# Kernel optimization log

Measured on AMD Instinct MI355X. Metric: run time of the kernel, lower is better.

## Reference

```python
import jax, jax.numpy as jnp
import numpy as np

N_NODES = 100000
D_FEAT = 128
UNITS = 128
N_EDGES = 600000


def setup_inputs() -> dict:
    key = jax.random.key(0)
    k1, k2, k3, k4, k5 = jax.random.split(key, 5)
    X = jax.random.normal(k1, (N_NODES, D_FEAT), dtype=jnp.float32)
    ref_a = jax.random.randint(k2, (N_EDGES,), 0, N_NODES, dtype=jnp.int32)
    ref_b = jax.random.randint(k3, (N_EDGES,), 0, N_NODES, dtype=jnp.int32)
    # Glorot-ish scaled dense weights
    W_hidden = jax.random.normal(k4, (D_FEAT, UNITS), dtype=jnp.float32) * (1.0 / np.sqrt(D_FEAT))
    W_out = jax.random.normal(k5, (UNITS, UNITS), dtype=jnp.float32) * (1.0 / np.sqrt(UNITS))
    b_hidden = jnp.zeros((UNITS,), dtype=jnp.float32)
    b_out = jnp.zeros((UNITS,), dtype=jnp.float32)
    return dict(X=X, ref_a=ref_a, ref_b=ref_b, W_hidden=W_hidden,
                b_hidden=b_hidden, W_out=W_out, b_out=b_out)


def wl1_convolution(X, ref_a, ref_b):
    # WL1 neighborhood aggregation over undirected edges (ref_a, ref_b):
    # each node keeps its own features plus the sum of its neighbors'.
    n = X.shape[0]
    agg_a = jax.ops.segment_sum(X[ref_b], ref_a, num_segments=n)  # [N, D]
    agg_b = jax.ops.segment_sum(X[ref_a], ref_b, num_segments=n)  # [N, D]
    return X + agg_a + agg_b


def reference(X, ref_a, ref_b, W_hidden, b_hidden, W_out, b_out):
    X_agg = wl1_convolution(X, ref_a, ref_b)                 # [N, D]
    X_hid = jax.nn.relu(X_agg @ W_hidden + b_hidden)          # [N, U] (inner_activation=relu)
    X_out = X_hid @ W_out + b_out                             # [N, U] (activation=linear)
    return X_out
```

## Files before the change

### kernel.cpp

```cpp
#include <hip/hip_runtime.h>

#define CAP 64

typedef short bf16x8 __attribute__((ext_vector_type(8)));
typedef float f32x4 __attribute__((ext_vector_type(4)));
typedef unsigned short u16;
typedef unsigned int u32;

__device__ __forceinline__ u16 f32_to_bf16(float f) {
  u32 b = __float_as_uint(f);
  b += 0x7fffu + ((b >> 16) & 1u);
  return (u16)(b >> 16);
}

__global__ void convert_x_kernel(const float* __restrict__ X,
                                 u16* __restrict__ Xb, int n8) {
  int i = blockIdx.x * blockDim.x + threadIdx.x;
  if (i >= n8) return;
  float4 a = ((const float4*)X)[2 * i];
  float4 b = ((const float4*)X)[2 * i + 1];
  int4 o;
  o.x = (int)((u32)f32_to_bf16(a.x) | ((u32)f32_to_bf16(a.y) << 16));
  o.y = (int)((u32)f32_to_bf16(a.z) | ((u32)f32_to_bf16(a.w) << 16));
  o.z = (int)((u32)f32_to_bf16(b.x) | ((u32)f32_to_bf16(b.y) << 16));
  o.w = (int)((u32)f32_to_bf16(b.z) | ((u32)f32_to_bf16(b.w) << 16));
  ((int4*)Xb)[i] = o;
}

__global__ __launch_bounds__(256) void fill_adj_xcd_kernel(
    const int* __restrict__ ra, const int* __restrict__ rb,
    int* __restrict__ cnt, int* __restrict__ adj, int nedges, int nx) {
  const int myx = blockIdx.x & 7;
  const int slice = blockIdx.x >> 3;
  int t = slice * 256 + threadIdx.x;
  int e0 = t * 2;
  if (e0 >= nedges) return;
  bool has1 = (e0 + 1) < nedges;
  long long apk = __builtin_nontemporal_load((const long long*)ra + t);
  long long bpk = __builtin_nontemporal_load((const long long*)rb + t);
  int2 av = make_int2((int)apk, (int)(apk >> 32));
  int2 bv = make_int2((int)bpk, (int)(bpk >> 32));

  int d[4], s[4];
  d[0] = av.x; s[0] = bv.x;
  d[1] = bv.x; s[1] = av.x;
  d[2] = has1 ? av.y : -1; s[2] = bv.y;
  d[3] = has1 ? bv.y : -1; s[3] = av.y;
#pragma unroll
  for (int i = 0; i < 4; ++i) {
    if (d[i] >= 0 && (d[i] & 7) == myx) {
      int bkt = myx * nx + (d[i] >> 3);
      int p = atomicAdd(&cnt[bkt], 1);
      if (p < CAP) adj[(size_t)bkt * CAP + p] = s[i];
    }
  }
}

__global__ void gather_agg_kernel(const u16* __restrict__ Xb,
                                  const int* __restrict__ cnt,
                                  int* __restrict__ adj,
                                  int nnodes, int nx) {
  int gid = blockIdx.x * blockDim.x + threadIdx.x;
  int wid = gid >> 6;
  int l = gid & 63;
  int half = l >> 5;
  int hl = l & 31;
  int node = wid * 2 + half;
  if (node >= nnodes) return;
  const uint2* Xv = (const uint2*)Xb;
  const int bkt = (node & 7) * nx + (node >> 3);
  const int* lst = adj + (size_t)bkt * CAP;
  int n = cnt[bkt];
  if (n > CAP) n = CAP;
  int idx0 = lst[hl];
  int idx1 = (n > 32) ? lst[hl + 32] : 0;
  uint2 ps = Xv[(size_t)node * 32 + hl];
  float a0 = __uint_as_float(ps.x << 16);
  float a1 = __uint_as_float(ps.x & 0xffff0000u);
  float a2 = __uint_as_float(ps.y << 16);
  float a3 = __uint_as_float(ps.y & 0xffff0000u);
  const int base = half << 5;
  for (int k = 0; k < n; k += 8) {
    uint2 pv[8];
#pragma unroll
    for (int t = 0; t < 8; ++t) {
      int pos = k + t;
      int sel = (pos < 32) ? idx0 : idx1;
      int nb = __shfl(sel, base + (pos & 31));
      pv[t] = (pos < n) ? Xv[(size_t)nb * 32 + hl] : make_uint2(0u, 0u);
    }
#pragma unroll
    for (int t = 0; t < 8; ++t) {
      a0 += __uint_as_float(pv[t].x << 16);
      a1 += __uint_as_float(pv[t].x & 0xffff0000u);
      a2 += __uint_as_float(pv[t].y << 16);
      a3 += __uint_as_float(pv[t].y & 0xffff0000u);
    }
  }
  u32 w0 = (u32)f32_to_bf16(a0) | ((u32)f32_to_bf16(a1) << 16);
  u32 w1 = (u32)f32_to_bf16(a2) | ((u32)f32_to_bf16(a3) << 16);
  ((uint2*)adj)[(size_t)bkt * 32 + hl] = make_uint2(w0, w1);
}

__global__ void convert_w_kernel(const float* __restrict__ Wh,
                                 const float* __restrict__ Wo,
                                 u16* __restrict__ WhT,
                                 u16* __restrict__ WoT) {
  int idx = blockIdx.x * 256 + threadIdx.x;
  const float* src = (idx < 16384) ? Wh : Wo;
  u16* dst = (idx < 16384) ? WhT : WoT;
  int i = idx & 16383;
  int k = i >> 7, n = i & 127;
  dst[n * 128 + k] = f32_to_bf16(src[k * 128 + n]);
}

__global__ __launch_bounds__(256) void mlp_mfma_kernel(
    const u16* __restrict__ Xagg,
    const u16* __restrict__ WhT,
    const u16* __restrict__ WoT,
    const float* __restrict__ bh,
    const float* __restrict__ bo,
    float* __restrict__ out, int nnodes, int nx) {
  __shared__ u16 smem[2 * 128 * 128];
  u16* sA = smem;
  u16* sW = smem + 16384;

  const int tid = threadIdx.x;
  const int w = tid >> 6;
  const int l = tid & 63;
  const int l15 = l & 15;
  const int l4 = l >> 4;
  const int r0 = blockIdx.x * 128;

#pragma unroll
  for (int t = 0; t < 8; ++t) {
    int id = tid + t * 256;
    int r = id >> 4, u = id & 15;
    int gr = r0 + r;
    if (gr >= nnodes) gr = nnodes - 1;
    size_t xrow = (size_t)((gr & 7) * nx + (gr >> 3)) * 128;
    *(int4*)&sA[r * 128 + ((u ^ (r & 15)) * 8)] =
        *(const int4*)&Xagg[xrow + u * 8];
    *(int4*)&sW[r * 128 + ((u ^ (r & 15)) * 8)] =
        *(const int4*)&WhT[r * 128 + u * 8];
  }

  float bhv[8], bov[8];
#pragma unroll
  for (int j = 0; j < 8; ++j) {
    bhv[j] = bh[j * 16 + l15];
    bov[j] = bo[j * 16 + l15];
  }
  __syncthreads();

  const int m0 = w * 32 + l15;
  const int m1 = w * 32 + 16 + l15;

  f32x4 acc[2][8];
#pragma unroll
  for (int i = 0; i < 2; ++i)
#pragma unroll
    for (int j = 0; j < 8; ++j) acc[i][j] = (f32x4){0.f, 0.f, 0.f, 0.f};

#pragma unroll
  for (int c = 0; c < 4; ++c) {
    int pu = ((c * 4 + l4) ^ l15) * 8;
    bf16x8 a0 = *(bf16x8*)&sA[m0 * 128 + pu];
    bf16x8 a1 = *(bf16x8*)&sA[m1 * 128 + pu];
#pragma unroll
    for (int j = 0; j < 8; ++j) {
      bf16x8 bfr = *(bf16x8*)&sW[(j * 16 + l15) * 128 + pu];
      acc[0][j] = __builtin_amdgcn_mfma_f32_16x16x32_bf16(a0, bfr, acc[0][j], 0, 0, 0);
      acc[1][j] = __builtin_amdgcn_mfma_f32_16x16x32_bf16(a1, bfr, acc[1][j], 0, 0, 0);
    }
  }

  __syncthreads();

#pragma unroll
  for (int t = 0; t < 8; ++t) {
    int id = tid + t * 256;
    int r = id >> 4, u = id & 15;
    *(int4*)&sW[r * 128 + ((u ^ (r & 15)) * 8)] =
        *(const int4*)&WoT[r * 128 + u * 8];
  }

#pragma unroll
  for (int i = 0; i < 2; ++i)
#pragma unroll
    for (int j = 0; j < 8; ++j)
#pragma unroll
      for (int r = 0; r < 4; ++r) {
        int m = w * 32 + i * 16 + l4 * 4 + r;
        float v = fmaxf(acc[i][j][r] + bhv[j], 0.f);
        int k = j * 16 + l15;
        sA[m * 128 + (((k >> 3) ^ (m & 15)) * 8) + (k & 7)] = f32_to_bf16(v);
      }
  __syncthreads();

#pragma unroll
  for (int i = 0; i < 2; ++i)
#pragma unroll
    for (int j = 0; j < 8; ++j) acc[i][j] = (f32x4){0.f, 0.f, 0.f, 0.f};

#pragma unroll
  for (int c = 0; c < 4; ++c) {
    int pu = ((c * 4 + l4) ^ l15) * 8;
    bf16x8 a0 = *(bf16x8*)&sA[m0 * 128 + pu];
    bf16x8 a1 = *(bf16x8*)&sA[m1 * 128 + pu];
#pragma unroll
    for (int j = 0; j < 8; ++j) {
      bf16x8 bfr = *(bf16x8*)&sW[(j * 16 + l15) * 128 + pu];
      acc[0][j] = __builtin_amdgcn_mfma_f32_16x16x32_bf16(a0, bfr, acc[0][j], 0, 0, 0);
      acc[1][j] = __builtin_amdgcn_mfma_f32_16x16x32_bf16(a1, bfr, acc[1][j], 0, 0, 0);
    }
  }

  __syncthreads();

  float* sOut = (float*)smem;
#pragma unroll
  for (int i = 0; i < 2; ++i)
#pragma unroll
    for (int j = 0; j < 8; ++j)
#pragma unroll
      for (int r = 0; r < 4; ++r) {
        int m = w * 32 + i * 16 + l4 * 4 + r;
        sOut[m * 128 + j * 16 + l15] = acc[i][j][r] + bov[j];
      }
  __syncthreads();
#pragma unroll
  for (int t = 0; t < 16; ++t) {
    int id = tid + t * 256;
    int r = id >> 5, u4 = id & 31;
    int gr = r0 + r;
    if (gr < nnodes)
      ((float4*)out)[(size_t)gr * 32 + u4] = ((const float4*)sOut)[id];
  }
}

extern "C" void kernel_launch(void* const* d_in, const int* in_sizes, int n_in,
                              void* d_out, int out_size, void* d_ws,
                              size_t ws_size, hipStream_t stream) {
  const float* X = (const float*)d_in[0];
  const int* ra = (const int*)d_in[1];
  const int* rb = (const int*)d_in[2];
  const float* Wh = (const float*)d_in[3];
  const float* bh = (const float*)d_in[4];
  const float* Wo = (const float*)d_in[5];
  const float* bo = (const float*)d_in[6];
  float* out = (float*)d_out;

  int nnodes = in_sizes[0] / 128;
  int nedges = in_sizes[1];
  int nx = (nnodes + 7) / 8;

  int* cnt = (int*)d_ws;
  int* adj = cnt + (size_t)nx * 8;
  u16* WhT = (u16*)d_ws;
  u16* WoT = WhT + 16384;
  u16* Xb = (u16*)d_out;

  int n8 = nnodes * 16;
  hipMemsetAsync(cnt, 0, (size_t)nx * 8 * 4, stream);
  convert_x_kernel<<<(n8 + 255) / 256, 256, 0, stream>>>(X, Xb, n8);
  int nslices = ((nedges + 1) / 2 + 255) / 256;
  fill_adj_xcd_kernel<<<nslices * 8, 256, 0, stream>>>(ra, rb, cnt, adj,
                                                       nedges, nx);
  int nwaves = (nnodes + 1) / 2;
  gather_agg_kernel<<<(nwaves * 64 + 255) / 256, 256, 0, stream>>>(
      Xb, cnt, adj, nnodes, nx);
  convert_w_kernel<<<128, 256, 0, stream>>>(Wh, Wo, WhT, WoT);
  mlp_mfma_kernel<<<(nnodes + 127) / 128, 256, 0, stream>>>(
      (const u16*)adj, WhT, WoT, bh, bo, out, nnodes, nx);
}
```

Baseline: 230.6 us.

## Bind adjacency fill to hardware XCD with persistent work queue and workgroup-scope atomics

The adjacency build reads the XCC_ID hardware register so each persistent block handles only destinations owned by its own XCD. Blocks pull edge slices from a per-XCD atomic queue, and a sweep kernel afterwards processes any slices left unclaimed. Because each XCD's counters are touched only by blocks on that XCD, the counter increments use relaxed workgroup-scope atomics instead of device-scope ones, which is meant to keep the atomics in the local L2 and avoid cross-die coherence. The correctness of this depends on an undocumented assumption: workgroup scope is treated as coherent across all CUs of one XCD. It also adds a queue-claim atomic and two barriers per slice, plus an extra kernel launch.

```diff
diff --git a/kernel.cpp b/kernel.cpp
--- a/kernel.cpp
+++ b/kernel.cpp
@@ -27,11 +27,11 @@
   ((int4*)Xb)[i] = o;
 }
 
-__global__ __launch_bounds__(256) void fill_adj_xcd_kernel(
+template <bool WG>
+__device__ __forceinline__ void process_slice(
     const int* __restrict__ ra, const int* __restrict__ rb,
-    int* __restrict__ cnt, int* __restrict__ adj, int nedges, int nx) {
-  const int myx = blockIdx.x & 7;
-  const int slice = blockIdx.x >> 3;
+    int* __restrict__ cnt_f, int* __restrict__ adj_f, int nedges, int slice,
+    int myx) {
   int t = slice * 256 + threadIdx.x;
   int e0 = t * 2;
   if (e0 >= nedges) return;
@@ -49,17 +49,55 @@
 #pragma unroll
   for (int i = 0; i < 4; ++i) {
     if (d[i] >= 0 && (d[i] & 7) == myx) {
-      int bkt = myx * nx + (d[i] >> 3);
-      int p = atomicAdd(&cnt[bkt], 1);
-      if (p < CAP) adj[(size_t)bkt * CAP + p] = s[i];
-    }
-  }
+      int b = d[i] >> 3;
+      int p;
+      if (WG)
+        p = __hip_atomic_fetch_add(&cnt_f[b], 1, __ATOMIC_RELAXED,
+                                   __HIP_MEMORY_SCOPE_WORKGROUP);
+      else
+        p = atomicAdd(&cnt_f[b], 1);
+      if (p < CAP) adj_f[(size_t)b * CAP + p] = s[i];
+    }
+  }
+}
+
+__global__ __launch_bounds__(256) void fill_adj_fast_kernel(
+    const int* __restrict__ ra, const int* __restrict__ rb,
+    int* __restrict__ q, int* __restrict__ cnt, int* __restrict__ adj,
+    int nedges, int nx, int nxc, int nslices) {
+  __shared__ int s_slice;
+  int x;
+  asm volatile("s_getreg_b32 %0, hwreg(HW_REG_XCC_ID)" : "=s"(x));
+  x &= 7;
+  int* cnt_f = cnt + (size_t)x * nxc;
+  int* adj_f = adj + (size_t)x * nx * CAP;
+  for (;;) {
+    if (threadIdx.x == 0) s_slice = atomicAdd(&q[x], 1);
+    __syncthreads();
+    int slice = s_slice;
+    __syncthreads();
+    if (slice >= nslices) break;
+    process_slice<true>(ra, rb, cnt_f, adj_f, nedges, slice, x);
+  }
+}
+
+__global__ __launch_bounds__(256) void fill_adj_sweep_kernel(
+    const int* __restrict__ ra, const int* __restrict__ rb,
+    const int* __restrict__ q, int* __restrict__ cnt, int* __restrict__ adj,
+    int nedges, int nx, int nxc, int nslices) {
+  int f = blockIdx.x;
+  int* cnt_f = cnt + (size_t)f * nxc;
+  int* adj_f = adj + (size_t)f * nx * CAP;
+  int start = q[f];
+  if (start > nslices) start = nslices;
+  for (int s = start; s < nslices; ++s)
+    process_slice<false>(ra, rb, cnt_f, adj_f, nedges, s, f);
 }
 
 __global__ void gather_agg_kernel(const u16* __restrict__ Xb,
                                   const int* __restrict__ cnt,
                                   int* __restrict__ adj,
-                                  int nnodes, int nx) {
+                                  int nnodes, int nx, int nxc) {
   int gid = blockIdx.x * blockDim.x + threadIdx.x;
   int wid = gid >> 6;
   int l = gid & 63;
@@ -68,9 +106,10 @@
   int node = wid * 2 + half;
   if (node >= nnodes) return;
   const uint2* Xv = (const uint2*)Xb;
-  const int bkt = (node & 7) * nx + (node >> 3);
+  const int f = node & 7, v = node >> 3;
+  const int bkt = f * nx + v;
   const int* lst = adj + (size_t)bkt * CAP;
-  int n = cnt[bkt];
+  int n = cnt[(size_t)f * nxc + v];
   if (n > CAP) n = CAP;
   int idx0 = lst[hl];
   int idx1 = (n > 32) ? lst[hl + 32] : 0;
@@ -254,22 +293,26 @@
   int nnodes = in_sizes[0] / 128;
   int nedges = in_sizes[1];
   int nx = (nnodes + 7) / 8;
-
-  int* cnt = (int*)d_ws;
-  int* adj = cnt + (size_t)nx * 8;
+  int nxc = (nx + 15) & ~15;
+
+  int* q = (int*)d_ws;
+  int* cnt = q + 16;
+  int* adj = cnt + (size_t)8 * nxc;
   u16* WhT = (u16*)d_ws;
   u16* WoT = WhT + 16384;
   u16* Xb = (u16*)d_out;
 
   int n8 = nnodes * 16;
-  hipMemsetAsync(cnt, 0, (size_t)nx * 8 * 4, stream);
+  hipMemsetAsync(d_ws, 0, (size_t)(16 + 8 * nxc) * 4, stream);
   convert_x_kernel<<<(n8 + 255) / 256, 256, 0, stream>>>(X, Xb, n8);
   int nslices = ((nedges + 1) / 2 + 255) / 256;
-  fill_adj_xcd_kernel<<<nslices * 8, 256, 0, stream>>>(ra, rb, cnt, adj,
-                                                       nedges, nx);
+  fill_adj_fast_kernel<<<2048, 256, 0, stream>>>(ra, rb, q, cnt, adj, nedges,
+                                                 nx, nxc, nslices);
+  fill_adj_sweep_kernel<<<8, 256, 0, stream>>>(ra, rb, q, cnt, adj, nedges,
+                                               nx, nxc, nslices);
   int nwaves = (nnodes + 1) / 2;
   gather_agg_kernel<<<(nwaves * 64 + 255) / 256, 256, 0, stream>>>(
-      Xb, cnt, adj, nnodes, nx);
+      Xb, cnt, adj, nnodes, nx, nxc);
   convert_w_kernel<<<128, 256, 0, stream>>>(Wh, Wo, WhT, WoT);
   mlp_mfma_kernel<<<(nnodes + 127) / 128, 256, 0, stream>>>(
       (const u16*)adj, WhT, WoT, bh, bo, out, nnodes, nx);
```

Result: slower. 328.7 us (+42.5%).
